# Optimization experiments

Measured on AMD Instinct MI355X. Metric: run time of the kernel, lower is better.

Reference implementation:

```python
import jax, jax.numpy as jnp
import numpy as np

GAMMA = 0.01
INFER_STEP = 3


def softor(x, axis, gamma=GAMMA):
    # smoothed logic-OR: gamma*logsumexp(x/gamma), normalized if it exceeds 1 (alphailp/NSFR semantics)
    lse = gamma * jax.nn.logsumexp(x / gamma, axis=axis)
    m = jnp.max(lse)
    return jnp.where(m > 1.0, lse / m, lse)


def clause_eval(R, I, gamma=GAMMA):
    # R: [C,B,G] per-clause valuations, I: [C,G,S,L] index tensor (values in [0,G))
    # gathered[c,b,g,s,l] = R[c, b, I[c,g,s,l]]
    gathered = jax.vmap(lambda Rc, Ic: jnp.take(Rc, Ic, axis=1))(R, I)  # [C,B,G,S,L]
    body = jnp.prod(gathered, axis=-1)  # product over body atoms L -> [C,B,G,S]
    return softor(body, axis=-1, gamma=gamma)  # soft-OR over substitutions S -> [C,B,G]


def setup_inputs() -> dict:
    key = jax.random.key(0)
    k1, k2 = jax.random.split(key)
    C, B, G, S, L = 4, 128, 2048, 32, 3
    x = jax.random.uniform(k1, (B, G), dtype=jnp.float32)  # atom valuations in [0,1]
    I = jax.random.randint(k2, (C, G, S, L), 0, G, dtype=jnp.int32)
    return {"x": x, "I": I}


def reference(x, I):
    C = I.shape[0]
    B, G = x.shape
    R = jnp.broadcast_to(x[None], (C, B, G))  # expand to per-clause valuation
    for _ in range(INFER_STEP):
        # amalgamate previous valuation with one inference step via soft-OR along stacked dim
        R = softor(jnp.stack([R, clause_eval(R, I)], axis=1), axis=1)
    return R
```

## Files before the change

kernel.cpp:

```cpp
#include <hip/hip_runtime.h>
#include <cstdint>
#include <cstddef>

#define C_ 4
#define B_ 128
#define G_ 2048
#define S_ 32
#define L_ 3
#define NSTEP_ 3
#define GAMMA_ 0.01f
#define INVG_LOG2E_ 144.26950408889634f
#define GAMMA_LN2_ 0.0069314718055994530942f

__device__ __forceinline__ float slot_max(const uint32_t* slots, int slot) {
  float m = 0.0f;
#pragma unroll
  for (int k = 0; k < 8; ++k)
    m = fmaxf(m, __uint_as_float(slots[slot * 128 + k * 16]));
  return m;
}

__global__ __launch_bounds__(256) void k_initT(const float* __restrict__ x,
                                               float* __restrict__ xT) {
  __shared__ float tile[32][33];
  const int g0 = blockIdx.x * 32, b0 = blockIdx.y * 32;
  const int tx = threadIdx.x;
  for (int i = threadIdx.y; i < 32; i += 8)
    tile[i][tx] = x[(size_t)(b0 + i) * G_ + g0 + tx];
  __syncthreads();
  for (int j = threadIdx.y; j < 32; j += 8)
    xT[(size_t)(g0 + j) * B_ + b0 + tx] = tile[tx][j];
}

__global__ __launch_bounds__(128) void k_gather(
    const float* __restrict__ Abase, size_t cstride,
    const int* __restrict__ Idx, float* __restrict__ Lout,
    uint32_t* slots, int prev_slot, int out_slot) {
  __shared__ int sidx[S_ * L_];
  __shared__ float wmax[2];
  const int tid = threadIdx.x;
  const int bid = blockIdx.x;
  const int cg = ((bid & 7) << 10) | (bid >> 3);
  const int c = cg >> 11;

  if (tid < S_ * L_) sidx[tid] = Idx[(size_t)cg * (S_ * L_) + tid];
  const float mprev = slot_max(slots, prev_slot);
  const float scale = (mprev > 1.0f) ? (1.0f / mprev) : 1.0f;
  const float s3 = scale * scale * scale;
  const float K = s3 * INVG_LOG2E_;
  __syncthreads();

  const float* Ac = Abase + (size_t)c * cstride + tid;

  float M = -1.0f;
  float acc = 0.0f;
#pragma unroll
  for (int s0 = 0; s0 < S_; s0 += 8) {
    float v[24];
#pragma unroll
    for (int j = 0; j < 24; ++j)
      v[j] = Ac[(size_t)sidx[s0 * 3 + j] * B_];
    float b[8];
#pragma unroll
    for (int k = 0; k < 8; ++k) b[k] = v[3 * k] * v[3 * k + 1] * v[3 * k + 2];
    float cm = b[0];
#pragma unroll
    for (int k = 1; k < 8; ++k) cm = fmaxf(cm, b[k]);
    const float Mn = fmaxf(M, cm);
    acc *= exp2f((M - Mn) * K);
#pragma unroll
    for (int k = 0; k < 8; ++k) acc += exp2f((b[k] - Mn) * K);
    M = Mn;
  }
  const float lse = M * s3 + GAMMA_LN2_ * log2f(acc);
  Lout[(size_t)cg * B_ + tid] = lse;

  float t = lse;
#pragma unroll
  for (int off = 32; off >= 1; off >>= 1) t = fmaxf(t, __shfl_xor(t, off));
  if ((tid & 63) == 0) wmax[tid >> 6] = t;
  __syncthreads();
  if (tid == 0)
    atomicMax(slots + out_slot * 128 + (bid & 7) * 16,
              __float_as_uint(fmaxf(wmax[0], wmax[1])));
}

__global__ __launch_bounds__(256) void k_elem(
    const float* __restrict__ Rin, size_t rstride, float* __restrict__ A,
    const float* __restrict__ Lin, uint32_t* slots, int prev_slot,
    int m1_slot, int out_slot) {
  __shared__ float wmax[4];
  const float mprev = slot_max(slots, prev_slot);
  const float sprev = (mprev > 1.0f) ? (1.0f / mprev) : 1.0f;
  const float m1 = slot_max(slots, m1_slot);
  const float s1 = (m1 > 1.0f) ? (1.0f / m1) : 1.0f;

  const int e = (blockIdx.x * 256 + threadIdx.x) * 4;
  const int c = e >> 18;
  const int rem = e & (G_ * B_ - 1);
  const float4 Rv =
      *reinterpret_cast<const float4*>(Rin + (size_t)c * rstride + rem);
  const float4 Lv = *reinterpret_cast<const float4*>(Lin + e);

  float r[4] = {Rv.x, Rv.y, Rv.z, Rv.w};
  float l[4] = {Lv.x, Lv.y, Lv.z, Lv.w};
  float o[4];
  float tmax = 0.0f;
#pragma unroll
  for (int k = 0; k < 4; ++k) {
    const float R = r[k] * sprev;
    const float ce = l[k] * s1;
    const float M = fmaxf(R, ce);
    const float mn = fminf(R, ce);
    const float lse2 =
        M + GAMMA_LN2_ * log2f(1.0f + exp2f((mn - M) * INVG_LOG2E_));
    o[k] = lse2;
    tmax = fmaxf(tmax, lse2);
  }
  *reinterpret_cast<float4*>(A + e) = make_float4(o[0], o[1], o[2], o[3]);

  float t = tmax;
#pragma unroll
  for (int off = 32; off >= 1; off >>= 1) t = fmaxf(t, __shfl_xor(t, off));
  if ((threadIdx.x & 63) == 0) wmax[threadIdx.x >> 6] = t;
  __syncthreads();
  if (threadIdx.x == 0) {
    const float bm = fmaxf(fmaxf(wmax[0], wmax[1]), fmaxf(wmax[2], wmax[3]));
    atomicMax(slots + out_slot * 128 + (blockIdx.x & 7) * 16,
              __float_as_uint(bm));
  }
}

__global__ __launch_bounds__(256) void k_out(const float* __restrict__ A,
                                             float* __restrict__ out,
                                             const uint32_t* __restrict__ slots,
                                             int mslot) {
  __shared__ float tile[32][33];
  const float mfin = slot_max(slots, mslot);
  const float sc = (mfin > 1.0f) ? (1.0f / mfin) : 1.0f;
  const int g0 = blockIdx.x * 32, b0 = blockIdx.y * 32, c = blockIdx.z;
  const int tx = threadIdx.x;
  for (int j = threadIdx.y; j < 32; j += 8)
    tile[j][tx] = A[((size_t)c * G_ + g0 + j) * B_ + b0 + tx];
  __syncthreads();
  for (int i = threadIdx.y; i < 32; i += 8)
    out[((size_t)c * B_ + b0 + i) * G_ + g0 + tx] = tile[tx][i] * sc;
}

extern "C" void kernel_launch(void* const* d_in, const int* in_sizes, int n_in,
                              void* d_out, int out_size, void* d_ws,
                              size_t ws_size, hipStream_t stream) {
  const float* x = (const float*)d_in[0];
  const int* Idx = (const int*)d_in[1];
  float* out = (float*)d_out;

  char* ws = (char*)d_ws;
  uint32_t* slots = (uint32_t*)ws;
  float* A = (float*)(ws + 4096);
  float* Lb = (float*)(ws + 4096 + (size_t)C_ * G_ * B_ * 4);
  float* xT = (float*)(ws + 4096 + (size_t)C_ * G_ * B_ * 8);

  hipMemsetAsync(slots, 0, 4096, stream);

  k_initT<<<dim3(G_ / 32, B_ / 32), dim3(32, 8), 0, stream>>>(x, xT);

  const size_t CS = (size_t)G_ * B_;
  for (int step = 0; step < NSTEP_; ++step) {
    const int prev = 2 * step;
    const int m1s = 2 * step + 1;
    const int m2s = 2 * step + 2;
    const float* Rsrc = (step == 0) ? xT : A;
    const size_t rs = (step == 0) ? 0 : CS;
    k_gather<<<C_ * G_, 128, 0, stream>>>(Rsrc, rs, Idx, Lb, slots, prev, m1s);
    k_elem<<<(C_ * G_ * B_) / (256 * 4), 256, 0, stream>>>(Rsrc, rs, A, Lb,
                                                           slots, prev, m1s,
                                                           m2s);
  }

  k_out<<<dim3(G_ / 32, B_ / 32, C_), dim3(32, 8), 0, stream>>>(A, out, slots,
                                                                2 * NSTEP_);
}
```

Baseline: 169.3 us.

## Gather from fp16 copy of valuations with one wave per ground atom

Keeps a half-precision shadow copy of the valuations, written by the transpose and elementwise kernels. The gather kernel reads it with packed half2 loads and assigns one 64-lane wave per ground atom, each lane handling two batch columns. It also uses readfirstlane for the indices and removes the block-level reduction barrier. Halving the bytes per random row gather is meant to cut the bandwidth and latency of the gather. The cost is fp16 rounding of the valuations before the product and the steep exp2 scaling by 1/gamma, which may move results beyond tolerance, plus extra fp16 stores.

```diff
diff --git a/kernel.cpp b/kernel.cpp
--- a/kernel.cpp
+++ b/kernel.cpp
@@ -1,4 +1,5 @@
 #include <hip/hip_runtime.h>
+#include <hip/hip_fp16.h>
 #include <cstdint>
 #include <cstddef>
 
@@ -12,83 +13,111 @@
 #define INVG_LOG2E_ 144.26950408889634f
 #define GAMMA_LN2_ 0.0069314718055994530942f
 
+#define SLOT_U_ 256
+#define BANK_U_ 32
 __device__ __forceinline__ float slot_max(const uint32_t* slots, int slot) {
   float m = 0.0f;
 #pragma unroll
   for (int k = 0; k < 8; ++k)
-    m = fmaxf(m, __uint_as_float(slots[slot * 128 + k * 16]));
+    m = fmaxf(m, __uint_as_float(slots[slot * SLOT_U_ + k * BANK_U_]));
   return m;
 }
 
 __global__ __launch_bounds__(256) void k_initT(const float* __restrict__ x,
-                                               float* __restrict__ xT) {
+                                               float* __restrict__ xT,
+                                               __half* __restrict__ x16) {
   __shared__ float tile[32][33];
   const int g0 = blockIdx.x * 32, b0 = blockIdx.y * 32;
   const int tx = threadIdx.x;
   for (int i = threadIdx.y; i < 32; i += 8)
     tile[i][tx] = x[(size_t)(b0 + i) * G_ + g0 + tx];
   __syncthreads();
-  for (int j = threadIdx.y; j < 32; j += 8)
-    xT[(size_t)(g0 + j) * B_ + b0 + tx] = tile[tx][j];
+  for (int j = threadIdx.y; j < 32; j += 8) {
+    const float v = tile[tx][j];
+    xT[(size_t)(g0 + j) * B_ + b0 + tx] = v;
+    x16[(size_t)(g0 + j) * B_ + b0 + tx] = __float2half_rn(v);
+  }
 }
 
 __global__ __launch_bounds__(128) void k_gather(
-    const float* __restrict__ Abase, size_t cstride,
+    const __half* __restrict__ A16, size_t cstride,
     const int* __restrict__ Idx, float* __restrict__ Lout,
     uint32_t* slots, int prev_slot, int out_slot) {
-  __shared__ int sidx[S_ * L_];
-  __shared__ float wmax[2];
+  __shared__ int sidx[2 * S_ * L_];
   const int tid = threadIdx.x;
+  const int lane = tid & 63;
+  const int w = tid >> 6;
   const int bid = blockIdx.x;
-  const int cg = ((bid & 7) << 10) | (bid >> 3);
+  const int cgp = ((bid & 7) << 9) | (bid >> 3);
+  const int cg = 2 * cgp + w;
   const int c = cg >> 11;
 
-  if (tid < S_ * L_) sidx[tid] = Idx[(size_t)cg * (S_ * L_) + tid];
+  for (int i = tid; i < 2 * S_ * L_; i += 128)
+    sidx[i] = Idx[(size_t)(2 * cgp) * (S_ * L_) + i];
   const float mprev = slot_max(slots, prev_slot);
   const float scale = (mprev > 1.0f) ? (1.0f / mprev) : 1.0f;
   const float s3 = scale * scale * scale;
   const float K = s3 * INVG_LOG2E_;
   __syncthreads();
 
-  const float* Ac = Abase + (size_t)c * cstride + tid;
-
-  float M = -1.0f;
-  float acc = 0.0f;
+  const int* widx = sidx + w * (S_ * L_);
+  const __half* Ac = A16 + (size_t)c * cstride;
+
+  float M0 = -1.0f, M1 = -1.0f;
+  float acc0 = 0.0f, acc1 = 0.0f;
 #pragma unroll
   for (int s0 = 0; s0 < S_; s0 += 8) {
-    float v[24];
-#pragma unroll
-    for (int j = 0; j < 24; ++j)
-      v[j] = Ac[(size_t)sidx[s0 * 3 + j] * B_];
-    float b[8];
-#pragma unroll
-    for (int k = 0; k < 8; ++k) b[k] = v[3 * k] * v[3 * k + 1] * v[3 * k + 2];
-    float cm = b[0];
-#pragma unroll
-    for (int k = 1; k < 8; ++k) cm = fmaxf(cm, b[k]);
-    const float Mn = fmaxf(M, cm);
-    acc *= exp2f((M - Mn) * K);
-#pragma unroll
-    for (int k = 0; k < 8; ++k) acc += exp2f((b[k] - Mn) * K);
-    M = Mn;
-  }
-  const float lse = M * s3 + GAMMA_LN2_ * log2f(acc);
-  Lout[(size_t)cg * B_ + tid] = lse;
-
-  float t = lse;
+    __half2 v[24];
+#pragma unroll
+    for (int j = 0; j < 24; ++j) {
+      const int row = __builtin_amdgcn_readfirstlane(widx[s0 * 3 + j]);
+      v[j] =
+          *reinterpret_cast<const __half2*>(Ac + (size_t)row * B_ + 2 * lane);
+    }
+    float b0[8], b1[8];
+#pragma unroll
+    for (int k = 0; k < 8; ++k) {
+      const float2 f0 = __half22float2(v[3 * k + 0]);
+      const float2 f1 = __half22float2(v[3 * k + 1]);
+      const float2 f2 = __half22float2(v[3 * k + 2]);
+      b0[k] = f0.x * f1.x * f2.x;
+      b1[k] = f0.y * f1.y * f2.y;
+    }
+    float cm0 = b0[0], cm1 = b1[0];
+#pragma unroll
+    for (int k = 1; k < 8; ++k) {
+      cm0 = fmaxf(cm0, b0[k]);
+      cm1 = fmaxf(cm1, b1[k]);
+    }
+    const float Mn0 = fmaxf(M0, cm0);
+    const float Mn1 = fmaxf(M1, cm1);
+    acc0 *= exp2f((M0 - Mn0) * K);
+    acc1 *= exp2f((M1 - Mn1) * K);
+#pragma unroll
+    for (int k = 0; k < 8; ++k) {
+      acc0 += exp2f((b0[k] - Mn0) * K);
+      acc1 += exp2f((b1[k] - Mn1) * K);
+    }
+    M0 = Mn0;
+    M1 = Mn1;
+  }
+  const float lse0 = M0 * s3 + GAMMA_LN2_ * log2f(acc0);
+  const float lse1 = M1 * s3 + GAMMA_LN2_ * log2f(acc1);
+  *reinterpret_cast<float2*>(Lout + (size_t)cg * B_ + 2 * lane) =
+      make_float2(lse0, lse1);
+
+  float t = fmaxf(lse0, lse1);
 #pragma unroll
   for (int off = 32; off >= 1; off >>= 1) t = fmaxf(t, __shfl_xor(t, off));
-  if ((tid & 63) == 0) wmax[tid >> 6] = t;
-  __syncthreads();
-  if (tid == 0)
-    atomicMax(slots + out_slot * 128 + (bid & 7) * 16,
-              __float_as_uint(fmaxf(wmax[0], wmax[1])));
+  if (lane == 0)
+    atomicMax(slots + out_slot * SLOT_U_ + (bid & 7) * BANK_U_,
+              __float_as_uint(t));
 }
 
 __global__ __launch_bounds__(256) void k_elem(
     const float* __restrict__ Rin, size_t rstride, float* __restrict__ A,
-    const float* __restrict__ Lin, uint32_t* slots, int prev_slot,
-    int m1_slot, int out_slot) {
+    __half* __restrict__ A16, const float* __restrict__ Lin, uint32_t* slots,
+    int prev_slot, int m1_slot, int out_slot) {
   __shared__ float wmax[4];
   const float mprev = slot_max(slots, prev_slot);
   const float sprev = (mprev > 1.0f) ? (1.0f / mprev) : 1.0f;
@@ -118,6 +147,15 @@
     tmax = fmaxf(tmax, lse2);
   }
   *reinterpret_cast<float4*>(A + e) = make_float4(o[0], o[1], o[2], o[3]);
+  if (A16) {
+    union {
+      __half2 h[2];
+      uint2 u;
+    } pk;
+    pk.h[0] = __floats2half2_rn(o[0], o[1]);
+    pk.h[1] = __floats2half2_rn(o[2], o[3]);
+    *reinterpret_cast<uint2*>(A16 + e) = pk.u;
+  }
 
   float t = tmax;
 #pragma unroll
@@ -126,7 +164,7 @@
   __syncthreads();
   if (threadIdx.x == 0) {
     const float bm = fmaxf(fmaxf(wmax[0], wmax[1]), fmaxf(wmax[2], wmax[3]));
-    atomicMax(slots + out_slot * 128 + (blockIdx.x & 7) * 16,
+    atomicMax(slots + out_slot * SLOT_U_ + (blockIdx.x & 7) * BANK_U_,
               __float_as_uint(bm));
   }
 }
@@ -154,27 +192,32 @@
   const int* Idx = (const int*)d_in[1];
   float* out = (float*)d_out;
 
+  const size_t CS = (size_t)G_ * B_;
   char* ws = (char*)d_ws;
   uint32_t* slots = (uint32_t*)ws;
-  float* A = (float*)(ws + 4096);
-  float* Lb = (float*)(ws + 4096 + (size_t)C_ * G_ * B_ * 4);
-  float* xT = (float*)(ws + 4096 + (size_t)C_ * G_ * B_ * 8);
-
-  hipMemsetAsync(slots, 0, 4096, stream);
-
-  k_initT<<<dim3(G_ / 32, B_ / 32), dim3(32, 8), 0, stream>>>(x, xT);
-
-  const size_t CS = (size_t)G_ * B_;
+  float* A = (float*)(ws + 16384);
+  float* Lb = A + CS * C_;
+  float* xT = Lb + CS * C_;
+  __half* A16 = (__half*)(xT + CS);
+  __half* x16 = A16 + CS * C_;
+
+  hipMemsetAsync(slots, 0, 8192, stream);
+
+  k_initT<<<dim3(G_ / 32, B_ / 32), dim3(32, 8), 0, stream>>>(x, xT, x16);
+
   for (int step = 0; step < NSTEP_; ++step) {
     const int prev = 2 * step;
     const int m1s = 2 * step + 1;
     const int m2s = 2 * step + 2;
+    const __half* Gsrc = (step == 0) ? x16 : A16;
+    const size_t gs = (step == 0) ? 0 : CS;
     const float* Rsrc = (step == 0) ? xT : A;
     const size_t rs = (step == 0) ? 0 : CS;
-    k_gather<<<C_ * G_, 128, 0, stream>>>(Rsrc, rs, Idx, Lb, slots, prev, m1s);
-    k_elem<<<(C_ * G_ * B_) / (256 * 4), 256, 0, stream>>>(Rsrc, rs, A, Lb,
-                                                           slots, prev, m1s,
-                                                           m2s);
+    __half* A16out = (step < NSTEP_ - 1) ? A16 : nullptr;
+    k_gather<<<(C_ * G_) / 2, 128, 0, stream>>>(Gsrc, gs, Idx, Lb, slots, prev,
+                                                m1s);
+    k_elem<<<(C_ * G_ * B_) / (256 * 4), 256, 0, stream>>>(
+        Rsrc, rs, A, A16out, Lb, slots, prev, m1s, m2s);
   }
 
   k_out<<<dim3(G_ / 32, B_ / 32, C_), dim3(32, 8), 0, stream>>>(A, out, slots,
```

After: 154.9 us. 1.09x faster.
